# Kernel optimization log

Hardware: AMD Instinct MI355X
Metric: run time of the kernel (lower is better)

Reference implementation:

```python
import jax, jax.numpy as jnp
import numpy as np

N, F_IN, H, OUT = 8192, 512, 128, 3
DEG_P = 16.0 / N  # avg degree ~16


def setup_inputs() -> dict:
    key = jax.random.key(0)
    ks = jax.random.split(key, 10)
    x = jax.random.normal(ks[0], (N, F_IN), dtype=jnp.float32)
    adj = (jax.random.uniform(ks[1], (N, N)) < DEG_P).astype(jnp.float32)

    def glorot(k, shape):
        lim = float(np.sqrt(6.0 / (shape[0] + shape[1])))
        return jax.random.uniform(k, shape, jnp.float32, -lim, lim)

    return {
        "x": x,
        "adj": adj,
        "Wl1": glorot(ks[2], (F_IN, H)),   # neighbor-agg weight, layer 1
        "Wr1": glorot(ks[3], (F_IN, H)),   # root/self weight, layer 1
        "b1": jnp.zeros((H,), jnp.float32),
        "Wl2": glorot(ks[4], (H, H)),
        "Wr2": glorot(ks[5], (H, H)),
        "b2": jnp.zeros((H,), jnp.float32),
        "Wd": glorot(ks[6], (H, OUT)),
        "bd": jnp.zeros((OUT,), jnp.float32),
    }


def _sage(x, adj, Wl, Wr, b):
    # GraphSAGE-mean: mean over neighbors via dense adjacency, then transform.
    deg = jnp.maximum(adj.sum(axis=1, keepdims=True), 1.0)  # [N,1]
    agg = (adj @ x) / deg                                    # [N,F]
    return agg @ Wl + x @ Wr + b


def _cdist(y):
    # pairwise Euclidean distances, grad-safe sqrt (zero grad on zero dist)
    sq = jnp.sum(y * y, axis=-1)                             # [N]
    d2 = jnp.maximum(sq[:, None] + sq[None, :] - 2.0 * (y @ y.T), 0.0)
    return jnp.where(d2 > 0, jnp.sqrt(jnp.where(d2 > 0, d2, 1.0)), 0.0)


def reference(x, adj, Wl1, Wr1, b1, Wl2, Wr2, b2, Wd, bd):
    h = jax.nn.relu(_sage(x, adj, Wl1, Wr1, b1))
    # dropout p=0.5 is identity in eval mode
    h = _sage(h, adj, Wl2, Wr2, b2)
    y = h @ Wd + bd                                          # [N,3]
    return _cdist(y)                                         # [N,N]
```

## Files before the change

### kernel.cpp

```cpp
#include <hip/hip_runtime.h>
#include <math.h>

#define NN 8192
#define FIN 512
#define HD 128
#define CAP 128

typedef float f32x4 __attribute__((ext_vector_type(4)));

__global__ __launch_bounds__(256) void k_front(
    const float* __restrict__ x, const float* __restrict__ Wl1,
    const float* __restrict__ Wr1, const float* __restrict__ adj,
    const float* __restrict__ Wl2, const float* __restrict__ Wr2,
    const float* __restrict__ b2, const float* __restrict__ Wd,
    const float* __restrict__ bd,
    float* __restrict__ xl, float* __restrict__ xr,
    int* __restrict__ nbr, int* __restrict__ degi, float* __restrict__ degf,
    float4* __restrict__ wsm)
{
    __shared__ float As[32][32];
    __shared__ float Bs[32][128];
    const int tid = threadIdx.x;
    const int b = blockIdx.x;

    if (b == 2560) {
        const int t = tid;
        if (t < HD) {
            float l0 = 0, l1 = 0, l2 = 0, r0 = 0, r1 = 0, r2 = 0;
            for (int c = 0; c < HD; ++c) {
                const float w0 = Wd[c * 3 + 0], w1 = Wd[c * 3 + 1], w2 = Wd[c * 3 + 2];
                const float wl = Wl2[t * HD + c];
                const float wr = Wr2[t * HD + c];
                l0 = fmaf(wl, w0, l0); l1 = fmaf(wl, w1, l1); l2 = fmaf(wl, w2, l2);
                r0 = fmaf(wr, w0, r0); r1 = fmaf(wr, w1, r1); r2 = fmaf(wr, w2, r2);
            }
            wsm[t]       = make_float4(l0, l1, l2, 0.f);
            wsm[128 + t] = make_float4(r0, r1, r2, 0.f);
            if (t == 0) {
                float c0 = bd[0], c1 = bd[1], c2 = bd[2];
                for (int c = 0; c < HD; ++c) {
                    c0 = fmaf(b2[c], Wd[c * 3 + 0], c0);
                    c1 = fmaf(b2[c], Wd[c * 3 + 1], c1);
                    c2 = fmaf(b2[c], Wd[c * 3 + 2], c2);
                }
                wsm[256] = make_float4(c0, c1, c2, 0.f);
            }
        }
    } else if (b % 5 == 0) {
        const int gi = b / 5;
        const float* W = (gi < 256) ? Wl1 : Wr1;
        float* Cout    = (gi < 256) ? xl  : xr;
        const int row0 = (gi & 255) * 32;
        const int rg = tid >> 5, cg = tid & 31;
        const int ar = tid >> 3, ak = (tid & 7) * 4;
        const int bk = tid >> 5, bc = (tid & 31) * 4;
        float acc[4][4] = {};
        for (int ch = 0; ch < FIN / 32; ++ch) {
            const int kc = ch * 32;
            __syncthreads();
            const float4 va = *(const float4*)(x + (size_t)(row0 + ar) * FIN + kc + ak);
            As[ak + 0][ar] = va.x; As[ak + 1][ar] = va.y;
            As[ak + 2][ar] = va.z; As[ak + 3][ar] = va.w;
            #pragma unroll
            for (int it = 0; it < 4; ++it)
                *(float4*)&Bs[bk + 8 * it][bc] =
                    *(const float4*)(W + (size_t)(kc + bk + 8 * it) * HD + bc);
            __syncthreads();
            #pragma unroll
            for (int k = 0; k < 32; ++k) {
                const float4 a4 = *(const float4*)&As[k][rg * 4];
                const float4 b4 = *(const float4*)&Bs[k][cg * 4];
                const float av[4] = {a4.x, a4.y, a4.z, a4.w};
                const float bv[4] = {b4.x, b4.y, b4.z, b4.w};
                #pragma unroll
                for (int a = 0; a < 4; ++a)
                    #pragma unroll
                    for (int bb = 0; bb < 4; ++bb)
                        acc[a][bb] = fmaf(av[a], bv[bb], acc[a][bb]);
            }
        }
        #pragma unroll
        for (int a = 0; a < 4; ++a)
            *(float4*)(Cout + (size_t)(row0 + rg * 4 + a) * HD + cg * 4) =
                make_float4(acc[a][0], acc[a][1], acc[a][2], acc[a][3]);
    } else {
        const int si = b - b / 5 - 1;
        const int w = tid >> 6, lane = tid & 63;
        const int i = si * 4 + w;
        int* lst = nbr + (size_t)i * CAP;
        const f32x4* row = (const f32x4*)(adj + (size_t)i * NN);
        const unsigned long long lmask = (1ull << lane) - 1ull;
        int cnt = 0;
        for (int it = 0; it < NN / 256; ++it) {
            const f32x4 a = __builtin_nontemporal_load(&row[it * 64 + lane]);
            const float vals[4] = {a.x, a.y, a.z, a.w};
            #pragma unroll
            for (int e = 0; e < 4; ++e) {
                const bool nz = (vals[e] != 0.0f);
                const unsigned long long m = __ballot(nz);
                if (nz) {
                    const int p = cnt + (int)__popcll(m & lmask);
                    if (p < CAP) lst[p] = (it * 64 + lane) * 4 + e;
                }
                cnt += (int)__popcll(m);
            }
        }
        if (lane == 0) {
            degi[i] = cnt < CAP ? cnt : CAP;
            degf[i] = fmaxf((float)cnt, 1.0f);
        }
    }
}

__global__ __launch_bounds__(256) void k_agg_proj(
    const float* __restrict__ xl, const float* __restrict__ xr,
    const float* __restrict__ b1, const int* __restrict__ nbr,
    const int* __restrict__ degi, const float* __restrict__ degf,
    const float4* __restrict__ wsm, float4* __restrict__ u4,
    float4* __restrict__ v4)
{
    __shared__ int lists[4][CAP];
    const int w = threadIdx.x >> 6, lane = threadIdx.x & 63;
    const int half = lane >> 5;
    const int cl = lane & 31;
    const int i = blockIdx.x * 4 + w;
    const int d = degi[i];
    const float inv = 1.0f / degf[i];
    const int* glst = nbr + (size_t)i * CAP;
    if (lane < d)      lists[w][lane]      = glst[lane];
    if (lane + 64 < d) lists[w][lane + 64] = glst[lane + 64];
    const int* lst = lists[w];

    f32x4 s = {0.f, 0.f, 0.f, 0.f};
    for (int t = 0; t < d; t += 8) {
        #pragma unroll
        for (int e = 0; e < 4; ++e) {
            const int idx = t + 2 * e + half;
            const bool ok = idx < d;
            const int j = ok ? lst[idx] : 0;
            const f32x4 a = ((const f32x4*)(xl + (size_t)j * HD))[cl];
            if (ok) s += a;
        }
    }
    s.x += __shfl_xor(s.x, 32);
    s.y += __shfl_xor(s.y, 32);
    s.z += __shfl_xor(s.z, 32);
    s.w += __shfl_xor(s.w, 32);

    const f32x4 rr = ((const f32x4*)(xr + (size_t)i * HD))[cl];
    const f32x4 bb = ((const f32x4*)b1)[cl];
    f32x4 h;
    h.x = fmaxf(fmaf(s.x, inv, rr.x + bb.x), 0.f);
    h.y = fmaxf(fmaf(s.y, inv, rr.y + bb.y), 0.f);
    h.z = fmaxf(fmaf(s.z, inv, rr.z + bb.z), 0.f);
    h.w = fmaxf(fmaf(s.w, inv, rr.w + bb.w), 0.f);

    const float4 w0 = wsm[cl * 4 + 0], w1 = wsm[cl * 4 + 1];
    const float4 w2 = wsm[cl * 4 + 2], w3 = wsm[cl * 4 + 3];
    const float4 q0 = wsm[128 + cl * 4 + 0], q1 = wsm[128 + cl * 4 + 1];
    const float4 q2 = wsm[128 + cl * 4 + 2], q3 = wsm[128 + cl * 4 + 3];
    float u0 = h.x * w0.x + h.y * w1.x + h.z * w2.x + h.w * w3.x;
    float u1 = h.x * w0.y + h.y * w1.y + h.z * w2.y + h.w * w3.y;
    float u2 = h.x * w0.z + h.y * w1.z + h.z * w2.z + h.w * w3.z;
    float v0 = h.x * q0.x + h.y * q1.x + h.z * q2.x + h.w * q3.x;
    float v1 = h.x * q0.y + h.y * q1.y + h.z * q2.y + h.w * q3.y;
    float v2 = h.x * q0.z + h.y * q1.z + h.z * q2.z + h.w * q3.z;
    #pragma unroll
    for (int off = 16; off; off >>= 1) {
        u0 += __shfl_xor(u0, off); u1 += __shfl_xor(u1, off); u2 += __shfl_xor(u2, off);
        v0 += __shfl_xor(v0, off); v1 += __shfl_xor(v1, off); v2 += __shfl_xor(v2, off);
    }
    if (lane == 0) {
        u4[i] = make_float4(u0, u1, u2, 0.f);
        v4[i] = make_float4(v0, v1, v2, 0.f);
    }
}

__global__ __launch_bounds__(256) void k_ycomb(
    const float4* __restrict__ u4, const float4* __restrict__ v4,
    const int* __restrict__ nbr, const int* __restrict__ degi,
    const float* __restrict__ degf, const float4* __restrict__ wsm,
    float4* __restrict__ y4)
{
    const int hw = threadIdx.x >> 5;
    const int lane = threadIdx.x & 31;
    const int i = blockIdx.x * 8 + hw;
    const int d = degi[i];
    const float inv = 1.0f / degf[i];
    const int* lst = nbr + (size_t)i * CAP;
    float s0 = 0.f, s1 = 0.f, s2 = 0.f;
    for (int base = 0; base + lane < d; base += 32) {
        const float4 u = u4[lst[base + lane]];
        s0 += u.x; s1 += u.y; s2 += u.z;
    }
    #pragma unroll
    for (int off = 16; off; off >>= 1) {
        s0 += __shfl_xor(s0, off); s1 += __shfl_xor(s1, off); s2 += __shfl_xor(s2, off);
    }
    if (lane == 0) {
        const float4 v = v4[i];
        const float4 c = wsm[256];
        y4[i] = make_float4(fmaf(s0, inv, v.x + c.x),
                            fmaf(s1, inv, v.y + c.y),
                            fmaf(s2, inv, v.z + c.z), 0.f);
    }
}

__global__ __launch_bounds__(256) void k_cdist(
    const float4* __restrict__ y4, float* __restrict__ out)
{
    __shared__ float4 yis[32];
    const int t = threadIdx.x;
    const int i0 = blockIdx.y * 32;
    if (t < 32) yis[t] = y4[i0 + t];
    __syncthreads();
    const int j0 = blockIdx.x * 1024 + t * 4;
    const float4 a0 = y4[j0 + 0], a1 = y4[j0 + 1];
    const float4 a2 = y4[j0 + 2], a3 = y4[j0 + 3];
    float* op = out + (size_t)i0 * NN + j0;
    #pragma unroll 4
    for (int ii = 0; ii < 32; ++ii) {
        const float4 yi = yis[ii];
        f32x4 r;
        { const float dx = yi.x - a0.x, dy = yi.y - a0.y, dz = yi.z - a0.z;
          r.x = sqrtf(fmaf(dx, dx, fmaf(dy, dy, dz * dz))); }
        { const float dx = yi.x - a1.x, dy = yi.y - a1.y, dz = yi.z - a1.z;
          r.y = sqrtf(fmaf(dx, dx, fmaf(dy, dy, dz * dz))); }
        { const float dx = yi.x - a2.x, dy = yi.y - a2.y, dz = yi.z - a2.z;
          r.z = sqrtf(fmaf(dx, dx, fmaf(dy, dy, dz * dz))); }
        { const float dx = yi.x - a3.x, dy = yi.y - a3.y, dz = yi.z - a3.z;
          r.w = sqrtf(fmaf(dx, dx, fmaf(dy, dy, dz * dz))); }
        __builtin_nontemporal_store(r, (f32x4*)op);
        op += NN;
    }
}

extern "C" void kernel_launch(void* const* d_in, const int* in_sizes, int n_in,
                              void* d_out, int out_size, void* d_ws, size_t ws_size,
                              hipStream_t stream) {
    const float* x   = (const float*)d_in[0];
    const float* adj = (const float*)d_in[1];
    const float* Wl1 = (const float*)d_in[2];
    const float* Wr1 = (const float*)d_in[3];
    const float* b1  = (const float*)d_in[4];
    const float* Wl2 = (const float*)d_in[5];
    const float* Wr2 = (const float*)d_in[6];
    const float* b2  = (const float*)d_in[7];
    const float* Wd  = (const float*)d_in[8];
    const float* bd  = (const float*)d_in[9];
    float* out = (float*)d_out;

    char* ws = (char*)d_ws;
    const size_t nbr_b  = (size_t)NN * CAP * 4;
    const size_t deg_b  = (size_t)NN * 4;
    const size_t vec_b  = (size_t)NN * 16;
    const size_t wsm_b  = 272 * 16;
    const size_t small_total = nbr_b + 2 * deg_b + 3 * vec_b + wsm_b;
    const size_t xl_b = (size_t)NN * HD * 4;

    size_t off = 0;
    int*    nbr  = (int*)(ws + off);    off += nbr_b;
    int*    degi = (int*)(ws + off);    off += deg_b;
    float*  degf = (float*)(ws + off);  off += deg_b;
    float4* u4   = (float4*)(ws + off); off += vec_b;
    float4* v4   = (float4*)(ws + off); off += vec_b;
    float4* y4   = (float4*)(ws + off); off += vec_b;
    float4* wsm  = (float4*)(ws + off); off += wsm_b;

    char* big = (ws_size >= small_total + 2 * xl_b) ? (ws + off) : (char*)d_out;
    float* xl = (float*)(big);
    float* xr = (float*)(big + xl_b);

    k_front<<<2561, 256, 0, stream>>>(
        x, Wl1, Wr1, adj, Wl2, Wr2, b2, Wd, bd,
        xl, xr, nbr, degi, degf, wsm);

    k_agg_proj<<<NN / 4, 256, 0, stream>>>(xl, xr, b1, nbr, degi, degf,
                                           wsm, u4, v4);

    k_ycomb<<<NN / 8, 256, 0, stream>>>(u4, v4, nbr, degi, degf, wsm, y4);

    k_cdist<<<dim3(NN / 1024, NN / 32), 256, 0, stream>>>(y4, out);
}
```

Measured before the change: 146.6 us.

## Move adjacency scan into aggregation kernel and fold bias into root GEMM

The adjacency row scan that builds neighbor lists moves out of the combined front kernel and into the aggregation kernel. Each wave now scans its row, keeps the list in shared memory and aggregates right away, instead of writing the list to global memory and reading it back in a second kernel. The front kernel becomes a plain GEMM plus the weight-precompute block, and the b1 bias is added into xr during the GEMM epilogue. The trade-off is that the dense 256MB adjacency scan no longer overlaps with the GEMM blocks, since the two now run serially in separate kernels.

```diff
diff --git a/kernel.cpp b/kernel.cpp
--- a/kernel.cpp
+++ b/kernel.cpp
@@ -8,14 +8,13 @@
 
 typedef float f32x4 __attribute__((ext_vector_type(4)));
 
-__global__ __launch_bounds__(256) void k_front(
+__global__ __launch_bounds__(256) void k_gemm(
     const float* __restrict__ x, const float* __restrict__ Wl1,
-    const float* __restrict__ Wr1, const float* __restrict__ adj,
+    const float* __restrict__ Wr1, const float* __restrict__ b1,
     const float* __restrict__ Wl2, const float* __restrict__ Wr2,
     const float* __restrict__ b2, const float* __restrict__ Wd,
     const float* __restrict__ bd,
     float* __restrict__ xl, float* __restrict__ xr,
-    int* __restrict__ nbr, int* __restrict__ degi, float* __restrict__ degf,
     float4* __restrict__ wsm)
 {
     __shared__ float As[32][32];
@@ -23,7 +22,7 @@
     const int tid = threadIdx.x;
     const int b = blockIdx.x;
 
-    if (b == 2560) {
+    if (b == 512) {
         const int t = tid;
         if (t < HD) {
             float l0 = 0, l1 = 0, l2 = 0, r0 = 0, r1 = 0, r2 = 0;
@@ -46,91 +45,86 @@
                 wsm[256] = make_float4(c0, c1, c2, 0.f);
             }
         }
-    } else if (b % 5 == 0) {
-        const int gi = b / 5;
-        const float* W = (gi < 256) ? Wl1 : Wr1;
-        float* Cout    = (gi < 256) ? xl  : xr;
-        const int row0 = (gi & 255) * 32;
-        const int rg = tid >> 5, cg = tid & 31;
-        const int ar = tid >> 3, ak = (tid & 7) * 4;
-        const int bk = tid >> 5, bc = (tid & 31) * 4;
-        float acc[4][4] = {};
-        for (int ch = 0; ch < FIN / 32; ++ch) {
-            const int kc = ch * 32;
-            __syncthreads();
-            const float4 va = *(const float4*)(x + (size_t)(row0 + ar) * FIN + kc + ak);
-            As[ak + 0][ar] = va.x; As[ak + 1][ar] = va.y;
-            As[ak + 2][ar] = va.z; As[ak + 3][ar] = va.w;
+        return;
+    }
+
+    const bool left = (b < 256);
+    const float* W = left ? Wl1 : Wr1;
+    float* Cout    = left ? xl  : xr;
+    const int row0 = (b & 255) * 32;
+    const int rg = tid >> 5, cg = tid & 31;
+    const int ar = tid >> 3, ak = (tid & 7) * 4;
+    const int bk = tid >> 5, bc = (tid & 31) * 4;
+    float acc[4][4] = {};
+    for (int ch = 0; ch < FIN / 32; ++ch) {
+        const int kc = ch * 32;
+        __syncthreads();
+        const float4 va = *(const float4*)(x + (size_t)(row0 + ar) * FIN + kc + ak);
+        As[ak + 0][ar] = va.x; As[ak + 1][ar] = va.y;
+        As[ak + 2][ar] = va.z; As[ak + 3][ar] = va.w;
+        #pragma unroll
+        for (int it = 0; it < 4; ++it)
+            *(float4*)&Bs[bk + 8 * it][bc] =
+                *(const float4*)(W + (size_t)(kc + bk + 8 * it) * HD + bc);
+        __syncthreads();
+        #pragma unroll
+        for (int k = 0; k < 32; ++k) {
+            const float4 a4 = *(const float4*)&As[k][rg * 4];
+            const float4 b4 = *(const float4*)&Bs[k][cg * 4];
+            const float av[4] = {a4.x, a4.y, a4.z, a4.w};
+            const float bv[4] = {b4.x, b4.y, b4.z, b4.w};
             #pragma unroll
-            for (int it = 0; it < 4; ++it)
-                *(float4*)&Bs[bk + 8 * it][bc] =
-                    *(const float4*)(W + (size_t)(kc + bk + 8 * it) * HD + bc);
-            __syncthreads();
-            #pragma unroll
-            for (int k = 0; k < 32; ++k) {
-                const float4 a4 = *(const float4*)&As[k][rg * 4];
-                const float4 b4 = *(const float4*)&Bs[k][cg * 4];
-                const float av[4] = {a4.x, a4.y, a4.z, a4.w};
-                const float bv[4] = {b4.x, b4.y, b4.z, b4.w};
+            for (int a = 0; a < 4; ++a)
                 #pragma unroll
-                for (int a = 0; a < 4; ++a)
-                    #pragma unroll
-                    for (int bb = 0; bb < 4; ++bb)
-                        acc[a][bb] = fmaf(av[a], bv[bb], acc[a][bb]);
-            }
-        }
-        #pragma unroll
-        for (int a = 0; a < 4; ++a)
-            *(float4*)(Cout + (size_t)(row0 + rg * 4 + a) * HD + cg * 4) =
-                make_float4(acc[a][0], acc[a][1], acc[a][2], acc[a][3]);
-    } else {
-        const int si = b - b / 5 - 1;
-        const int w = tid >> 6, lane = tid & 63;
-        const int i = si * 4 + w;
-        int* lst = nbr + (size_t)i * CAP;
-        const f32x4* row = (const f32x4*)(adj + (size_t)i * NN);
-        const unsigned long long lmask = (1ull << lane) - 1ull;
-        int cnt = 0;
-        for (int it = 0; it < NN / 256; ++it) {
-            const f32x4 a = __builtin_nontemporal_load(&row[it * 64 + lane]);
-            const float vals[4] = {a.x, a.y, a.z, a.w};
-            #pragma unroll
-            for (int e = 0; e < 4; ++e) {
-                const bool nz = (vals[e] != 0.0f);
-                const unsigned long long m = __ballot(nz);
-                if (nz) {
-                    const int p = cnt + (int)__popcll(m & lmask);
-                    if (p < CAP) lst[p] = (it * 64 + lane) * 4 + e;
-                }
-                cnt += (int)__popcll(m);
-            }
-        }
-        if (lane == 0) {
-            degi[i] = cnt < CAP ? cnt : CAP;
-            degf[i] = fmaxf((float)cnt, 1.0f);
-        }
-    }
-}
-
-__global__ __launch_bounds__(256) void k_agg_proj(
-    const float* __restrict__ xl, const float* __restrict__ xr,
-    const float* __restrict__ b1, const int* __restrict__ nbr,
-    const int* __restrict__ degi, const float* __restrict__ degf,
-    const float4* __restrict__ wsm, float4* __restrict__ u4,
-    float4* __restrict__ v4)
+                for (int bb = 0; bb < 4; ++bb)
+                    acc[a][bb] = fmaf(av[a], bv[bb], acc[a][bb]);
+        }
+    }
+    float4 bias = make_float4(0.f, 0.f, 0.f, 0.f);
+    if (!left) bias = ((const float4*)b1)[cg];
+    #pragma unroll
+    for (int a = 0; a < 4; ++a)
+        *(float4*)(Cout + (size_t)(row0 + rg * 4 + a) * HD + cg * 4) =
+            make_float4(acc[a][0] + bias.x, acc[a][1] + bias.y,
+                        acc[a][2] + bias.z, acc[a][3] + bias.w);
+}
+
+__global__ __launch_bounds__(256) void k_scanagg(
+    const float* __restrict__ adj, const float* __restrict__ xl,
+    const float* __restrict__ xrb, const float4* __restrict__ wsm,
+    int* __restrict__ nbr, int* __restrict__ degi, float* __restrict__ degf,
+    float4* __restrict__ u4, float4* __restrict__ v4)
 {
     __shared__ int lists[4][CAP];
     const int w = threadIdx.x >> 6, lane = threadIdx.x & 63;
+    const int i = blockIdx.x * 4 + w;
+    int* lst = lists[w];
+
+    const f32x4* row = (const f32x4*)(adj + (size_t)i * NN);
+    const unsigned long long lmask = (1ull << lane) - 1ull;
+    int cnt = 0;
+    for (int it = 0; it < NN / 256; ++it) {
+        const f32x4 a = __builtin_nontemporal_load(&row[it * 64 + lane]);
+        const float vals[4] = {a.x, a.y, a.z, a.w};
+        #pragma unroll
+        for (int e = 0; e < 4; ++e) {
+            const bool nz = (vals[e] != 0.0f);
+            const unsigned long long m = __ballot(nz);
+            if (nz) {
+                const int p = cnt + (int)__popcll(m & lmask);
+                if (p < CAP) lst[p] = (it * 64 + lane) * 4 + e;
+            }
+            cnt += (int)__popcll(m);
+        }
+    }
+    const int d = cnt < CAP ? cnt : CAP;
+    const float inv = 1.0f / fmaxf((float)cnt, 1.0f);
+    if (lane < d)      nbr[(size_t)i * CAP + lane]      = lst[lane];
+    if (lane + 64 < d) nbr[(size_t)i * CAP + lane + 64] = lst[lane + 64];
+    if (lane == 0) { degi[i] = d; degf[i] = fmaxf((float)cnt, 1.0f); }
+
     const int half = lane >> 5;
     const int cl = lane & 31;
-    const int i = blockIdx.x * 4 + w;
-    const int d = degi[i];
-    const float inv = 1.0f / degf[i];
-    const int* glst = nbr + (size_t)i * CAP;
-    if (lane < d)      lists[w][lane]      = glst[lane];
-    if (lane + 64 < d) lists[w][lane + 64] = glst[lane + 64];
-    const int* lst = lists[w];
-
     f32x4 s = {0.f, 0.f, 0.f, 0.f};
     for (int t = 0; t < d; t += 8) {
         #pragma unroll
@@ -147,13 +141,12 @@
     s.z += __shfl_xor(s.z, 32);
     s.w += __shfl_xor(s.w, 32);
 
-    const f32x4 rr = ((const f32x4*)(xr + (size_t)i * HD))[cl];
-    const f32x4 bb = ((const f32x4*)b1)[cl];
+    const f32x4 rr = ((const f32x4*)(xrb + (size_t)i * HD))[cl];
     f32x4 h;
-    h.x = fmaxf(fmaf(s.x, inv, rr.x + bb.x), 0.f);
-    h.y = fmaxf(fmaf(s.y, inv, rr.y + bb.y), 0.f);
-    h.z = fmaxf(fmaf(s.z, inv, rr.z + bb.z), 0.f);
-    h.w = fmaxf(fmaf(s.w, inv, rr.w + bb.w), 0.f);
+    h.x = fmaxf(fmaf(s.x, inv, rr.x), 0.f);
+    h.y = fmaxf(fmaf(s.y, inv, rr.y), 0.f);
+    h.z = fmaxf(fmaf(s.z, inv, rr.z), 0.f);
+    h.w = fmaxf(fmaf(s.w, inv, rr.w), 0.f);
 
     const float4 w0 = wsm[cl * 4 + 0], w1 = wsm[cl * 4 + 1];
     const float4 w2 = wsm[cl * 4 + 2], w3 = wsm[cl * 4 + 3];
@@ -268,15 +261,14 @@
     float4* wsm  = (float4*)(ws + off); off += wsm_b;
 
     char* big = (ws_size >= small_total + 2 * xl_b) ? (ws + off) : (char*)d_out;
-    float* xl = (float*)(big);
-    float* xr = (float*)(big + xl_b);
-
-    k_front<<<2561, 256, 0, stream>>>(
-        x, Wl1, Wr1, adj, Wl2, Wr2, b2, Wd, bd,
-        xl, xr, nbr, degi, degf, wsm);
-
-    k_agg_proj<<<NN / 4, 256, 0, stream>>>(xl, xr, b1, nbr, degi, degf,
-                                           wsm, u4, v4);
+    float* xl  = (float*)(big);
+    float* xrb = (float*)(big + xl_b);
+
+    k_gemm<<<513, 256, 0, stream>>>(x, Wl1, Wr1, b1, Wl2, Wr2, b2, Wd, bd,
+                                    xl, xrb, wsm);
+
+    k_scanagg<<<NN / 4, 256, 0, stream>>>(adj, xl, xrb, wsm,
+                                          nbr, degi, degf, u4, v4);
 
     k_ycomb<<<NN / 8, 256, 0, stream>>>(u4, v4, nbr, degi, degf, wsm, y4);
 
```

New measurement: 145.0 us. Within noise of the previous version (-1.1%).
